# Kernel optimization log

Hardware: AMD Instinct MI355X
Metric: run time of the kernel (lower is better)

Reference implementation:

```python
import jax, jax.numpy as jnp
import numpy as np

B, T, C = 8, 2048, 1024
HEAD = 64

def setup_inputs() -> dict:
    key = jax.random.key(0)
    k1, k2 = jax.random.split(key)
    x = jax.random.normal(k1, (B, T, C), dtype=jnp.float32)
    W_qkv = jax.random.normal(k2, (C, 3 * HEAD), dtype=jnp.float32) * (C ** -0.5)
    return {"x": x, "W_qkv": W_qkv}

def reference(x, W_qkv):
    # qkv projection (bias-free Linear): [B,T,3*HEAD]
    qkv = x @ W_qkv
    q, k, v = jnp.split(qkv, 3, axis=-1)  # each [B,T,HEAD]
    # scaled dot-product scores [B,T,T]
    dots = jnp.einsum('btd,bsd->bts', q, k) * (HEAD ** -0.5)
    # causal mask (tril == keep)
    Tq = x.shape[1]
    causal = jnp.tril(jnp.ones((Tq, Tq), dtype=bool))
    dots = jnp.where(causal, dots, -jnp.inf)
    attn = jax.nn.softmax(dots, axis=-1)
    # dropout p=0.0 (eval) -> identity
    out = jnp.einsum('bts,bsd->btd', attn, v)  # [B,T,HEAD]
    return out
```

## Files before the change

kernel.cpp:

```cpp
#include <hip/hip_runtime.h>
#include <stdint.h>

#define NB 8
#define NT 2048
#define NC 1024
#define HD 64

typedef __attribute__((ext_vector_type(8)))  short s16x8;
typedef __attribute__((ext_vector_type(4)))  float f32x4;
typedef __attribute__((ext_vector_type(16))) float f32x16;

__device__ inline ushort f2b(float f) {
    union { float f; uint32_t u; } c; c.f = f;
    uint32_t u = c.u;
    uint32_t r = (u + 0x7fffu + ((u >> 16) & 1u)) >> 16;
    return (ushort)r;
}

__device__ inline uint32_t cvt_pk_bf16(float lo, float hi) {
    uint32_t r;
    asm("v_cvt_pk_bf16_f32 %0, %1, %2" : "=v"(r) : "v"(lo), "v"(hi));
    return r;
}

__device__ inline void gload_lds16(const void* gsrc, void* lds) {
    __builtin_amdgcn_global_load_lds(
        (const __attribute__((address_space(1))) void*)gsrc,
        (__attribute__((address_space(3))) void*)lds, 16, 0, 0);
}

__global__ __launch_bounds__(256) void wprep(const float* __restrict__ W,
                                             ushort* __restrict__ wt) {
    int tid = blockIdx.x * 256 + threadIdx.x;
    int n = tid >> 10;
    int k = tid & 1023;
    float v = W[k * 192 + n];
    if (n < 64) v *= 0.125f * 1.4426950408889634f;
    wt[n * 1024 + k] = f2b(v);
}

__global__ __launch_bounds__(256, 2) void qkv_gemm(const float* __restrict__ x,
                                                   const ushort* __restrict__ wt,
                                                   ushort* __restrict__ qs,
                                                   ushort* __restrict__ kk,
                                                   ushort* __restrict__ vt) {
    __shared__ __align__(16) float  Al[4][1024];
    __shared__ __align__(16) ushort Wl[4][6144];

    const int tid = threadIdx.x;
    const int wv  = tid >> 6;
    const int ls  = tid & 63;
    const int r16 = ls & 15;
    const int hi4 = ls >> 4;
    const int row0 = blockIdx.x * 32;

    const int acb = ((ls & 7) * 16) ^ (((ls >> 3) & 3) << 5) ^ (((ls >> 5) & 1) << 4);
    const float* xsrc = x + (size_t)(row0 + wv * 8 + (ls >> 3)) * NC + (acb >> 2);
    const int wkc = (ls & 3) ^ ((ls >> 3) & 3);
    const ushort* wsrc[3];
#pragma unroll
    for (int j = 0; j < 3; ++j) {
        int c = wv * 3 + j;
        wsrc[j] = wt + (size_t)(c * 16 + (ls >> 2)) * 1024 + wkc * 8;
    }

    int aoff[2];
#pragma unroll
    for (int m = 0; m < 2; ++m) {
        int r = m * 16 + r16;
        aoff[m] = r * 128 + ((hi4 ^ (r & 3)) << 5) + (((r >> 2) & 1) << 4);
    }
    int boff[3];
#pragma unroll
    for (int nf = 0; nf < 3; ++nf) {
        int n = (wv * 3 + nf) * 16 + r16;
        boff[nf] = n * 64 + ((hi4 ^ ((n >> 1) & 3)) << 4);
    }

    f32x4 acc[2][3];
#pragma unroll
    for (int i = 0; i < 2; ++i)
#pragma unroll
        for (int j = 0; j < 3; ++j)
#pragma unroll
            for (int e = 0; e < 4; ++e) acc[i][j][e] = 0.f;

    auto STAGE = [&](int t) {
        int bb = t & 3;
        gload_lds16(xsrc + t * 32, &Al[bb][wv * 256]);
#pragma unroll
        for (int j = 0; j < 3; ++j)
            gload_lds16(wsrc[j] + t * 32, &Wl[bb][(wv * 3 + j) * 512]);
    };

    auto COMPUTE = [&](int bb) {
        s16x8 af[2], bf[3];
#pragma unroll
        for (int m = 0; m < 2; ++m) {
            float4 a0 = *(const float4*)((const char*)&Al[bb][0] + aoff[m]);
            float4 a1 = *(const float4*)((const char*)&Al[bb][0] + (aoff[m] ^ 16));
            union { uint32_t w[4]; s16x8 v; } pk;
            pk.w[0] = cvt_pk_bf16(a0.x, a0.y);
            pk.w[1] = cvt_pk_bf16(a0.z, a0.w);
            pk.w[2] = cvt_pk_bf16(a1.x, a1.y);
            pk.w[3] = cvt_pk_bf16(a1.z, a1.w);
            af[m] = pk.v;
        }
#pragma unroll
        for (int nf = 0; nf < 3; ++nf)
            bf[nf] = *(const s16x8*)((const char*)&Wl[bb][0] + boff[nf]);
#pragma unroll
        for (int m = 0; m < 2; ++m)
#pragma unroll
            for (int nf = 0; nf < 3; ++nf)
                acc[m][nf] = __builtin_amdgcn_mfma_f32_16x16x32_bf16(
                    af[m], bf[nf], acc[m][nf], 0, 0, 0);
    };

    STAGE(0); STAGE(1); STAGE(2);

    for (int t = 0; t < 29; ++t) {
        asm volatile("s_waitcnt vmcnt(8)" ::: "memory");
        __builtin_amdgcn_s_barrier();
        __builtin_amdgcn_sched_barrier(0);
        STAGE(t + 3);
        COMPUTE(t & 3);
    }
    asm volatile("s_waitcnt vmcnt(8)" ::: "memory");
    __builtin_amdgcn_s_barrier();
    __builtin_amdgcn_sched_barrier(0);
    COMPUTE(29 & 3);
    asm volatile("s_waitcnt vmcnt(4)" ::: "memory");
    __builtin_amdgcn_s_barrier();
    __builtin_amdgcn_sched_barrier(0);
    COMPUTE(30 & 3);
    asm volatile("s_waitcnt vmcnt(0)" ::: "memory");
    __builtin_amdgcn_s_barrier();
    __builtin_amdgcn_sched_barrier(0);
    COMPUTE(31 & 3);

    const int b = row0 >> 11;
#pragma unroll
    for (int m = 0; m < 2; ++m) {
        const int rbase = row0 + m * 16 + hi4 * 4;
#pragma unroll
        for (int nf = 0; nf < 3; ++nf) {
            int nfg = wv * 3 + nf;
            int colg = nfg * 16 + r16;
            f32x4 v = acc[m][nf];
            if (nfg < 4) {
#pragma unroll
                for (int j = 0; j < 4; ++j)
                    qs[(size_t)(rbase + j) * HD + colg] = f2b(v[j]);
            } else if (nfg < 8) {
#pragma unroll
                for (int j = 0; j < 4; ++j)
                    kk[(size_t)(rbase + j) * HD + (colg - 64)] = f2b(v[j]);
            } else {
                int d = colg - 128;
                union { ushort4 s; ushort u[4]; } pk;
#pragma unroll
                for (int j = 0; j < 4; ++j) pk.u[j] = f2b(v[j]);
                *(ushort4*)(&vt[((size_t)(b * 64 + d)) * NT + (rbase & (NT - 1))]) = pk.s;
            }
        }
    }
}

__global__ __launch_bounds__(256) void attn(const ushort* __restrict__ qs,
                                            const ushort* __restrict__ kk,
                                            const ushort* __restrict__ vt,
                                            float* __restrict__ out) {
    __shared__ float ob[4][64][33];
    __shared__ float ml[4][2][32];

    const int bid  = blockIdx.x;
    const int b    = bid & 7;
    const int tile = 63 - (bid >> 3);
    const int tid  = threadIdx.x;
    const int wv   = tid >> 6;
    const int l    = tid & 63;
    const int qcol = l & 31;
    const int hi   = l >> 5;
    const int r0   = tile * 32;

    const ushort* qb = qs + ((size_t)(b * NT + r0)) * HD;
    const ushort* kb = kk + (size_t)b * NT * HD;
    const ushort* vb = vt + (size_t)b * HD * NT;

    s16x8 qf[4];
#pragma unroll
    for (int c = 0; c < 4; ++c)
        qf[c] = *(const s16x8*)(qb + (size_t)qcol * HD + c * 16 + hi * 8);

    f32x16 o0, o1;
#pragma unroll
    for (int i = 0; i < 16; ++i) { o0[i] = 0.f; o1[i] = 0.f; }
    float m = -3.0e30f, lsum = 0.f;

    if (wv <= tile) {
        s16x8 kf[4], vf[4];
        {
            const ushort* kr = kb + (size_t)(wv * 32 + qcol) * HD;
#pragma unroll
            for (int c = 0; c < 4; ++c)
                kf[c] = *(const s16x8*)(kr + c * 16 + hi * 8);
#pragma unroll
            for (int dt = 0; dt < 2; ++dt)
#pragma unroll
                for (int kc = 0; kc < 2; ++kc)
                    vf[dt * 2 + kc] = *(const s16x8*)(vb + (size_t)(dt * 32 + qcol) * NT
                                                      + wv * 32 + kc * 16 + hi * 8);
        }

        for (int kt = wv; kt <= tile; kt += 4) {
            f32x16 s;
#pragma unroll
            for (int i = 0; i < 16; ++i) s[i] = 0.f;
#pragma unroll
            for (int c = 0; c < 4; ++c)
                s = __builtin_amdgcn_mfma_f32_32x32x16_bf16(kf[c], qf[c], s, 0, 0, 0);

            s16x8 kfn[4], vfn[4];
            const bool more = (kt + 4 <= tile);
            if (more) {
                const ushort* kr = kb + (size_t)((kt + 4) * 32 + qcol) * HD;
#pragma unroll
                for (int c = 0; c < 4; ++c)
                    kfn[c] = *(const s16x8*)(kr + c * 16 + hi * 8);
#pragma unroll
                for (int dt = 0; dt < 2; ++dt)
#pragma unroll
                    for (int kc = 0; kc < 2; ++kc)
                        vfn[dt * 2 + kc] = *(const s16x8*)(vb + (size_t)(dt * 32 + qcol) * NT
                                                           + (kt + 4) * 32 + kc * 16 + hi * 8);
            }

            const bool diag = (kt == tile);
            float p[16];
#pragma unroll
            for (int r = 0; r < 16; ++r) {
                int klocal = (r & 3) + 8 * (r >> 2) + 4 * hi;
                float sv = s[r];
                if (diag && klocal > qcol) sv = -3.0e30f;
                p[r] = sv;
            }
            float pmax = p[0];
#pragma unroll
            for (int r = 1; r < 16; ++r) pmax = fmaxf(pmax, p[r]);
            pmax = fmaxf(pmax, __shfl_xor(pmax, 32));
            float mnew = fmaxf(m, pmax);
            float corr = exp2f(m - mnew);
            m = mnew;
            float rs = 0.f;
#pragma unroll
            for (int r = 0; r < 16; ++r) { p[r] = exp2f(p[r] - mnew); rs += p[r]; }
            rs += __shfl_xor(rs, 32);
            lsum = lsum * corr + rs;
#pragma unroll
            for (int i = 0; i < 16; ++i) { o0[i] *= corr; o1[i] *= corr; }

#pragma unroll
            for (int kc = 0; kc < 2; ++kc) {
                int pb = kc * 8;
                uint32_t a0 = cvt_pk_bf16(p[pb + 0], p[pb + 1]);
                uint32_t a1 = cvt_pk_bf16(p[pb + 2], p[pb + 3]);
                uint32_t b0 = cvt_pk_bf16(p[pb + 4], p[pb + 5]);
                uint32_t b1 = cvt_pk_bf16(p[pb + 6], p[pb + 7]);
                uint32_t a0x = __shfl_xor(a0, 32);
                uint32_t a1x = __shfl_xor(a1, 32);
                uint32_t b0x = __shfl_xor(b0, 32);
                uint32_t b1x = __shfl_xor(b1, 32);
                union { uint32_t w[4]; s16x8 v; } frag;
                frag.w[0] = hi ? b0x : a0;
                frag.w[1] = hi ? b1x : a1;
                frag.w[2] = hi ? b0  : a0x;
                frag.w[3] = hi ? b1  : a1x;
                o0 = __builtin_amdgcn_mfma_f32_32x32x16_bf16(vf[0 * 2 + kc], frag.v, o0, 0, 0, 0);
                o1 = __builtin_amdgcn_mfma_f32_32x32x16_bf16(vf[1 * 2 + kc], frag.v, o1, 0, 0, 0);
            }

            if (more) {
#pragma unroll
                for (int c = 0; c < 4; ++c) kf[c] = kfn[c];
#pragma unroll
                for (int c = 0; c < 4; ++c) vf[c] = vfn[c];
            }
        }
    }

#pragma unroll
    for (int r = 0; r < 16; ++r) {
        int d = (r & 3) + 8 * (r >> 2) + 4 * hi;
        ob[wv][d][qcol]      = o0[r];
        ob[wv][d + 32][qcol] = o1[r];
    }
    if (hi == 0) {
        ml[wv][0][qcol] = m;
        ml[wv][1][qcol] = lsum;
    }
    __syncthreads();

    const int q  = tid >> 3;
    const int j0 = (tid & 7) * 8;
    float mw[4];
#pragma unroll
    for (int w = 0; w < 4; ++w) mw[w] = ml[w][0][q];
    float M = fmaxf(fmaxf(mw[0], mw[1]), fmaxf(mw[2], mw[3]));
    float sw[4]; float L = 0.f;
#pragma unroll
    for (int w = 0; w < 4; ++w) {
        sw[w] = exp2f(mw[w] - M);
        L += sw[w] * ml[w][1][q];
    }
    float invL = 1.0f / L;
    float vals[8];
#pragma unroll
    for (int j = 0; j < 8; ++j) {
        int d = j0 + j;
        float acc = 0.f;
#pragma unroll
        for (int w = 0; w < 4; ++w) acc += sw[w] * ob[w][d][q];
        vals[j] = acc * invL;
    }
    float* orow = out + ((size_t)(b * NT + r0 + q)) * HD + j0;
    *(float4*)(orow)     = make_float4(vals[0], vals[1], vals[2], vals[3]);
    *(float4*)(orow + 4) = make_float4(vals[4], vals[5], vals[6], vals[7]);
}

extern "C" void kernel_launch(void* const* d_in, const int* in_sizes, int n_in,
                              void* d_out, int out_size, void* d_ws, size_t ws_size,
                              hipStream_t stream) {
    const float* x = (const float*)d_in[0];
    const float* W = (const float*)d_in[1];
    float* out = (float*)d_out;

    ushort* qs = (ushort*)d_ws;
    ushort* kk = qs + (size_t)NB * NT * HD;
    ushort* vt = kk + (size_t)NB * NT * HD;
    ushort* wt = vt + (size_t)NB * NT * HD;

    wprep<<<768, 256, 0, stream>>>(W, wt);
    qkv_gemm<<<512, 256, 0, stream>>>(x, wt, qs, kk, vt);
    attn<<<512, 256, 0, stream>>>(qs, kk, vt, out);
}
```

Before: 58.50 us.

## Restructure QKV GEMM to 64-row tiles with register-staged padded LDS pipeline

Rewrites the QKV projection GEMM to process 64 rows per block with 512 threads. Tiles now span 64 k per stage. Direct global-to-LDS loads are replaced by register staging into padded LDS buffers, triple-buffered with loads issued three stages ahead. This halves the number of W tile reloads per row and the number of barriers per k step. In exchange it costs more registers, uses only 256 blocks (one per CU), and relies on padding rather than XOR swizzles to avoid LDS bank conflicts.

```diff
diff --git a/kernel.cpp b/kernel.cpp
--- a/kernel.cpp
+++ b/kernel.cpp
@@ -21,12 +21,6 @@
     uint32_t r;
     asm("v_cvt_pk_bf16_f32 %0, %1, %2" : "=v"(r) : "v"(lo), "v"(hi));
     return r;
-}
-
-__device__ inline void gload_lds16(const void* gsrc, void* lds) {
-    __builtin_amdgcn_global_load_lds(
-        (const __attribute__((address_space(1))) void*)gsrc,
-        (__attribute__((address_space(3))) void*)lds, 16, 0, 0);
 }
 
 __global__ __launch_bounds__(256) void wprep(const float* __restrict__ W,
@@ -39,43 +33,46 @@
     wt[n * 1024 + k] = f2b(v);
 }
 
-__global__ __launch_bounds__(256, 2) void qkv_gemm(const float* __restrict__ x,
+#define APITCH 272
+#define WPITCH 144
+
+__global__ __launch_bounds__(512, 1) void qkv_gemm(const float* __restrict__ x,
                                                    const ushort* __restrict__ wt,
                                                    ushort* __restrict__ qs,
                                                    ushort* __restrict__ kk,
                                                    ushort* __restrict__ vt) {
-    __shared__ __align__(16) float  Al[4][1024];
-    __shared__ __align__(16) ushort Wl[4][6144];
+    __shared__ __align__(16) char Al[3][64 * APITCH];
+    __shared__ __align__(16) char Wl[3][192 * WPITCH];
 
     const int tid = threadIdx.x;
     const int wv  = tid >> 6;
     const int ls  = tid & 63;
     const int r16 = ls & 15;
     const int hi4 = ls >> 4;
-    const int row0 = blockIdx.x * 32;
-
-    const int acb = ((ls & 7) * 16) ^ (((ls >> 3) & 3) << 5) ^ (((ls >> 5) & 1) << 4);
-    const float* xsrc = x + (size_t)(row0 + wv * 8 + (ls >> 3)) * NC + (acb >> 2);
-    const int wkc = (ls & 3) ^ ((ls >> 3) & 3);
-    const ushort* wsrc[3];
-#pragma unroll
-    for (int j = 0; j < 3; ++j) {
-        int c = wv * 3 + j;
-        wsrc[j] = wt + (size_t)(c * 16 + (ls >> 2)) * 1024 + wkc * 8;
-    }
+    const int g   = wv >> 2;
+    const int c   = wv & 3;
+    const int row0 = blockIdx.x * 64;
+
+    const int srow = ls >> 3;
+    const int sslt = ls & 7;
+    const float*  xA  = x + (size_t)(row0 + wv * 8 + srow) * NC + sslt * 4;
+    const ushort* wS0 = wt + (size_t)(wv * 24 + 0 + srow) * 1024 + sslt * 8;
+    const ushort* wS1 = wt + (size_t)(wv * 24 + 8 + srow) * 1024 + sslt * 8;
+    const ushort* wS2 = wt + (size_t)(wv * 24 + 16 + srow) * 1024 + sslt * 8;
+
+    const int aw  = (wv * 8 + srow) * APITCH + sslt * 16;
+    const int ww0 = (wv * 24 + 0 + srow) * WPITCH + sslt * 16;
+    const int ww1 = (wv * 24 + 8 + srow) * WPITCH + sslt * 16;
+    const int ww2 = (wv * 24 + 16 + srow) * WPITCH + sslt * 16;
 
     int aoff[2];
 #pragma unroll
-    for (int m = 0; m < 2; ++m) {
-        int r = m * 16 + r16;
-        aoff[m] = r * 128 + ((hi4 ^ (r & 3)) << 5) + (((r >> 2) & 1) << 4);
-    }
+    for (int m = 0; m < 2; ++m)
+        aoff[m] = (g * 32 + m * 16 + r16) * APITCH + hi4 * 32;
     int boff[3];
 #pragma unroll
-    for (int nf = 0; nf < 3; ++nf) {
-        int n = (wv * 3 + nf) * 16 + r16;
-        boff[nf] = n * 64 + ((hi4 ^ ((n >> 1) & 3)) << 4);
-    }
+    for (int nf = 0; nf < 3; ++nf)
+        boff[nf] = (c * 48 + nf * 16 + r16) * WPITCH + hi4 * 16;
 
     f32x4 acc[2][3];
 #pragma unroll
@@ -85,74 +82,83 @@
 #pragma unroll
             for (int e = 0; e < 4; ++e) acc[i][j][e] = 0.f;
 
-    auto STAGE = [&](int t) {
-        int bb = t & 3;
-        gload_lds16(xsrc + t * 32, &Al[bb][wv * 256]);
-#pragma unroll
-        for (int j = 0; j < 3; ++j)
-            gload_lds16(wsrc[j] + t * 32, &Wl[bb][(wv * 3 + j) * 512]);
+    struct Stage { float4 xa, xb; uint4 w0, w1, w2; };
+    Stage st[3];
+
+    auto LOADS = [&](int t, Stage& s) {
+        s.xa = *(const float4*)(xA + t * 64);
+        s.xb = *(const float4*)(xA + t * 64 + 32);
+        s.w0 = *(const uint4*)(wS0 + t * 64);
+        s.w1 = *(const uint4*)(wS1 + t * 64);
+        s.w2 = *(const uint4*)(wS2 + t * 64);
     };
-
+    auto WRITE = [&](int t, const Stage& s) {
+        int bb = t % 3;
+        *(float4*)(&Al[bb][aw])        = s.xa;
+        *(float4*)(&Al[bb][aw + 128])  = s.xb;
+        *(uint4*)(&Wl[bb][ww0]) = s.w0;
+        *(uint4*)(&Wl[bb][ww1]) = s.w1;
+        *(uint4*)(&Wl[bb][ww2]) = s.w2;
+    };
     auto COMPUTE = [&](int bb) {
-        s16x8 af[2], bf[3];
-#pragma unroll
-        for (int m = 0; m < 2; ++m) {
-            float4 a0 = *(const float4*)((const char*)&Al[bb][0] + aoff[m]);
-            float4 a1 = *(const float4*)((const char*)&Al[bb][0] + (aoff[m] ^ 16));
-            union { uint32_t w[4]; s16x8 v; } pk;
-            pk.w[0] = cvt_pk_bf16(a0.x, a0.y);
-            pk.w[1] = cvt_pk_bf16(a0.z, a0.w);
-            pk.w[2] = cvt_pk_bf16(a1.x, a1.y);
-            pk.w[3] = cvt_pk_bf16(a1.z, a1.w);
-            af[m] = pk.v;
+#pragma unroll
+        for (int kq = 0; kq < 2; ++kq) {
+            s16x8 af[2], bf[3];
+#pragma unroll
+            for (int m = 0; m < 2; ++m) {
+                const char* base = &Al[bb][0];
+                float4 a0 = *(const float4*)(base + aoff[m] + kq * 128);
+                float4 a1 = *(const float4*)(base + aoff[m] + kq * 128 + 16);
+                union { uint32_t w[4]; s16x8 v; } pk;
+                pk.w[0] = cvt_pk_bf16(a0.x, a0.y);
+                pk.w[1] = cvt_pk_bf16(a0.z, a0.w);
+                pk.w[2] = cvt_pk_bf16(a1.x, a1.y);
+                pk.w[3] = cvt_pk_bf16(a1.z, a1.w);
+                af[m] = pk.v;
+            }
+#pragma unroll
+            for (int nf = 0; nf < 3; ++nf)
+                bf[nf] = *(const s16x8*)(&Wl[bb][0] + boff[nf] + kq * 64);
+#pragma unroll
+            for (int m = 0; m < 2; ++m)
+#pragma unroll
+                for (int nf = 0; nf < 3; ++nf)
+                    acc[m][nf] = __builtin_amdgcn_mfma_f32_16x16x32_bf16(
+                        af[m], bf[nf], acc[m][nf], 0, 0, 0);
         }
-#pragma unroll
-        for (int nf = 0; nf < 3; ++nf)
-            bf[nf] = *(const s16x8*)((const char*)&Wl[bb][0] + boff[nf]);
-#pragma unroll
-        for (int m = 0; m < 2; ++m)
-#pragma unroll
-            for (int nf = 0; nf < 3; ++nf)
-                acc[m][nf] = __builtin_amdgcn_mfma_f32_16x16x32_bf16(
-                    af[m], bf[nf], acc[m][nf], 0, 0, 0);
     };
 
-    STAGE(0); STAGE(1); STAGE(2);
-
-    for (int t = 0; t < 29; ++t) {
-        asm volatile("s_waitcnt vmcnt(8)" ::: "memory");
+    LOADS(0, st[0]); LOADS(1, st[1]); LOADS(2, st[2]);
+    WRITE(0, st[0]);
+    __builtin_amdgcn_sched_barrier(0);
+    asm volatile("s_waitcnt lgkmcnt(0)" ::: "memory");
+    __builtin_amdgcn_s_barrier();
+    __builtin_amdgcn_sched_barrier(0);
+
+#pragma unroll
+    for (int t = 0; t < 16; ++t) {
+        if (t + 3 <= 15) LOADS(t + 3, st[(t + 3) % 3]);
+        if (t + 1 <= 15) WRITE(t + 1, st[(t + 1) % 3]);
+        __builtin_amdgcn_sched_barrier(0);
+        asm volatile("s_waitcnt lgkmcnt(0)" ::: "memory");
         __builtin_amdgcn_s_barrier();
         __builtin_amdgcn_sched_barrier(0);
-        STAGE(t + 3);
-        COMPUTE(t & 3);
-    }
-    asm volatile("s_waitcnt vmcnt(8)" ::: "memory");
-    __builtin_amdgcn_s_barrier();
-    __builtin_amdgcn_sched_barrier(0);
-    COMPUTE(29 & 3);
-    asm volatile("s_waitcnt vmcnt(4)" ::: "memory");
-    __builtin_amdgcn_s_barrier();
-    __builtin_amdgcn_sched_barrier(0);
-    COMPUTE(30 & 3);
-    asm volatile("s_waitcnt vmcnt(0)" ::: "memory");
-    __builtin_amdgcn_s_barrier();
-    __builtin_amdgcn_sched_barrier(0);
-    COMPUTE(31 & 3);
+        COMPUTE(t % 3);
+    }
 
     const int b = row0 >> 11;
 #pragma unroll
     for (int m = 0; m < 2; ++m) {
-        const int rbase = row0 + m * 16 + hi4 * 4;
+        const int rbase = row0 + g * 32 + m * 16 + hi4 * 4;
 #pragma unroll
         for (int nf = 0; nf < 3; ++nf) {
-            int nfg = wv * 3 + nf;
-            int colg = nfg * 16 + r16;
+            int colg = c * 48 + nf * 16 + r16;
             f32x4 v = acc[m][nf];
-            if (nfg < 4) {
+            if (colg < 64) {
 #pragma unroll
                 for (int j = 0; j < 4; ++j)
                     qs[(size_t)(rbase + j) * HD + colg] = f2b(v[j]);
-            } else if (nfg < 8) {
+            } else if (colg < 128) {
 #pragma unroll
                 for (int j = 0; j < 4; ++j)
                     kk[(size_t)(rbase + j) * HD + (colg - 64)] = f2b(v[j]);
@@ -341,6 +347,6 @@
     ushort* wt = vt + (size_t)NB * NT * HD;
 
     wprep<<<768, 256, 0, stream>>>(W, wt);
-    qkv_gemm<<<512, 256, 0, stream>>>(x, wt, qs, kk, vt);
+    qkv_gemm<<<256, 512, 0, stream>>>(x, wt, qs, kk, vt);
     attn<<<512, 256, 0, stream>>>(qs, kk, vt, out);
 }
```

Measured after the change: 100.0 us. +71.0%, slower.
